# Kernel tuning notes

Measured on AMD Instinct MI355X. Metric: run time of the kernel, lower is better.

The kernel has to match this reference:

```python
import jax, jax.numpy as jnp
import numpy as np

N, M, D = 65536, 1024, 2


def setup_inputs() -> dict:
    key = jax.random.key(0)
    k1, k2, k3 = jax.random.split(key, 3)
    sample = jax.random.uniform(k1, (N, D), dtype=jnp.float32)
    mu = jax.random.uniform(k2, (M, D), dtype=jnp.float32)
    # original init: A = 10 * I; add small noise so covariances are anisotropic
    A = 10.0 * jnp.broadcast_to(jnp.eye(D, dtype=jnp.float32), (M, D, D)) \
        + 0.1 * jax.random.normal(k3, (M, D, D), dtype=jnp.float32)
    w = jnp.ones((M, 1), dtype=jnp.float32)
    return {"sample": sample, "mu": mu, "A": A, "w": w}


def reference(sample, mu, A, w):
    # gamma_j = A_j @ A_j^T  -> precision matrices, (M, D, D)
    gamma = jnp.einsum('mde,mfe->mdf', A, A)
    # 2x2 determinant (only case implemented in the original module)
    det = gamma[:, 0, 0] * gamma[:, 1, 1] - gamma[:, 0, 1] * gamma[:, 1, 0]
    # log weights: log_softmax(w) + 0.5 * log det(gamma)
    log_w = jax.nn.log_softmax(w[:, 0], axis=0) + 0.5 * jnp.log(det)  # (M,)
    # Mahalanobis quadratic form q_ij = (x_i - mu_j)^T gamma_j (x_i - mu_j),
    # expanded to avoid materializing an (N, M, D) difference tensor.
    xGx = jnp.einsum('nd,mde,ne->nm', sample, gamma, sample)          # (N, M)
    gm = jnp.einsum('mde,me->md', gamma, mu)                          # (M, D)
    cross = sample @ gm.T                                             # (N, M)
    mGm = jnp.einsum('md,md->m', gm, mu)                              # (M,)
    q = xGx - 2.0 * cross + mGm[None, :]
    # log-likelihood per sample: logsumexp_j (log_w_j - q_ij)
    return jax.nn.logsumexp(log_w[None, :] - q, axis=1)               # (N,)
```

## Files before the change

kernel.cpp:

```cpp
#include <hip/hip_runtime.h>
#include <math.h>

#define LOG2E 1.4426950408889634f
#define LN2   0.6931471805599453f

static constexpr int M = 1024;
static constexpr int N = 65536;

__device__ inline float wave_max64(float v) {
    #pragma unroll
    for (int o = 32; o > 0; o >>= 1) v = fmaxf(v, __shfl_xor(v, o));
    return v;
}
__device__ inline float wave_sum64(float v) {
    #pragma unroll
    for (int o = 32; o > 0; o >>= 1) v += __shfl_xor(v, o);
    return v;
}

__global__ __launch_bounds__(1024)
void gm_all(const float* __restrict__ sample,
            const float* __restrict__ mu,
            const float* __restrict__ A,
            const float* __restrict__ w,
            float* __restrict__ out) {
    __shared__ __align__(16) float coef[M*6];
    __shared__ float partial[16*256];
    __shared__ float redA[16];
    __shared__ float redB[16];

    const int t    = threadIdx.x;
    const int lane = t & 63;
    const int wv   = t >> 6;
    const int base = blockIdx.x * 256;

    float x0[4], x1[4];
    #pragma unroll
    for (int k = 0; k < 4; k++) {
        const float2 p = ((const float2*)sample)[base + 64*k + lane];
        x0[k] = p.x; x1[k] = p.y;
    }

    const float4 a = ((const float4*)A)[t];
    const float g00 = a.x*a.x + a.y*a.y;
    const float g01 = a.x*a.z + a.y*a.w;
    const float g11 = a.z*a.z + a.w*a.w;
    const float2 m  = ((const float2*)mu)[t];
    const float gm0 = g00*m.x + g01*m.y;
    const float gm1 = g01*m.x + g11*m.y;
    const float mGm = gm0*m.x + gm1*m.y;
    const float det = g00*g11 - g01*g01;

    const float w2 = w[t] * LOG2E;
    const float t2 = w2 + 0.5f * __builtin_amdgcn_logf(det);

    float mw = wave_max64(w2);
    float mt = wave_max64(t2);
    if (lane == 0) { redA[wv] = mw; redB[wv] = mt; }
    __syncthreads();
    float wmax2 = redA[0], maxt2 = redB[0];
    #pragma unroll
    for (int i = 1; i < 16; i++) {
        wmax2 = fmaxf(wmax2, redA[i]);
        maxt2 = fmaxf(maxt2, redB[i]);
    }

    {
        float* c = coef + t*6;
        c[0] = t2 - maxt2 - LOG2E * mGm;
        c[1] = LOG2E * 2.0f * gm0;
        c[2] = LOG2E * 2.0f * gm1;
        c[3] = -LOG2E * g00;
        c[4] = -LOG2E * 2.0f * g01;
        c[5] = -LOG2E * g11;
    }
    __syncthreads();

    float sw = wave_sum64(__builtin_amdgcn_exp2f(w2 - wmax2));
    if (lane == 0) redA[wv] = sw;

    const float xx[4] = {x0[0]*x0[0], x0[1]*x0[1], x0[2]*x0[2], x0[3]*x0[3]};
    const float xy[4] = {x0[0]*x1[0], x0[1]*x1[1], x0[2]*x1[2], x0[3]*x1[3]};
    const float yy[4] = {x1[0]*x1[0], x1[1]*x1[1], x1[2]*x1[2], x1[3]*x1[3]};
    float accA[4] = {0.0f, 0.0f, 0.0f, 0.0f};
    float accB[4] = {0.0f, 0.0f, 0.0f, 0.0f};

    const float4* cw = (const float4*)(coef + wv*64*6);
    #pragma unroll 8
    for (int jj = 0; jj < 32; jj++) {
        const float4 q0 = cw[jj*3 + 0];
        const float4 q1 = cw[jj*3 + 1];
        const float4 q2 = cw[jj*3 + 2];
        #pragma unroll
        for (int k = 0; k < 4; k++) {
            const float va = fmaf(q1.y, yy[k], fmaf(q1.x, xy[k],
                             fmaf(q0.w, xx[k], fmaf(q0.z, x1[k],
                             fmaf(q0.y, x0[k], q0.x)))));
            const float vb = fmaf(q2.w, yy[k], fmaf(q2.z, xy[k],
                             fmaf(q2.y, xx[k], fmaf(q2.x, x1[k],
                             fmaf(q1.w, x0[k], q1.z)))));
            accA[k] += __builtin_amdgcn_exp2f(va);
            accB[k] += __builtin_amdgcn_exp2f(vb);
        }
    }

    #pragma unroll
    for (int k = 0; k < 4; k++)
        partial[wv*256 + 64*k + lane] = accA[k] + accB[k];
    __syncthreads();

    if (t < 256) {
        float s = 0.0f;
        #pragma unroll
        for (int w2i = 0; w2i < 16; w2i++) s += partial[w2i*256 + t];
        float se = 0.0f;
        #pragma unroll
        for (int i = 0; i < 16; i++) se += redA[i];
        const float lse2 = wmax2 + __builtin_amdgcn_logf(se);
        out[base + t] = LN2 * (maxt2 - lse2 + __builtin_amdgcn_logf(s));
    }
}

extern "C" void kernel_launch(void* const* d_in, const int* in_sizes, int n_in,
                              void* d_out, int out_size, void* d_ws, size_t ws_size,
                              hipStream_t stream) {
    const float* sample = (const float*)d_in[0];
    const float* mu     = (const float*)d_in[1];
    const float* A      = (const float*)d_in[2];
    const float* w      = (const float*)d_in[3];
    float* out = (float*)d_out;
    (void)d_ws; (void)ws_size;

    gm_all<<<N/256, 1024, 0, stream>>>(sample, mu, A, w, out);
}
```

Before: 72.85 us.

## Split coefficient prep into separate kernel and use packed FP32 FMA

```diff
diff --git a/kernel.cpp b/kernel.cpp
--- a/kernel.cpp
+++ b/kernel.cpp
@@ -6,6 +6,14 @@
 
 static constexpr int M = 1024;
 static constexpr int N = 65536;
+
+typedef float v2f __attribute__((ext_vector_type(2)));
+
+__device__ inline v2f pk_fma(v2f a, v2f b, v2f c) {
+    v2f d;
+    asm("v_pk_fma_f32 %0, %1, %2, %3" : "=v"(d) : "v"(a), "v"(b), "v"(c));
+    return d;
+}
 
 __device__ inline float wave_max64(float v) {
     #pragma unroll
@@ -19,27 +27,15 @@
 }
 
 __global__ __launch_bounds__(1024)
-void gm_all(const float* __restrict__ sample,
-            const float* __restrict__ mu,
-            const float* __restrict__ A,
-            const float* __restrict__ w,
-            float* __restrict__ out) {
-    __shared__ __align__(16) float coef[M*6];
-    __shared__ float partial[16*256];
+void gm_prep(const float* __restrict__ mu,
+             const float* __restrict__ A,
+             const float* __restrict__ w,
+             float* __restrict__ ws) {
     __shared__ float redA[16];
     __shared__ float redB[16];
-
     const int t    = threadIdx.x;
     const int lane = t & 63;
     const int wv   = t >> 6;
-    const int base = blockIdx.x * 256;
-
-    float x0[4], x1[4];
-    #pragma unroll
-    for (int k = 0; k < 4; k++) {
-        const float2 p = ((const float2*)sample)[base + 64*k + lane];
-        x0[k] = p.x; x1[k] = p.y;
-    }
 
     const float4 a = ((const float4*)A)[t];
     const float g00 = a.x*a.x + a.y*a.y;
@@ -64,60 +60,93 @@
         wmax2 = fmaxf(wmax2, redA[i]);
         maxt2 = fmaxf(maxt2, redB[i]);
     }
+    __syncthreads();
+    const float sw = wave_sum64(__builtin_amdgcn_exp2f(w2 - wmax2));
+    if (lane == 0) redA[wv] = sw;
+
+    float* c = ws + (t >> 1)*12 + (t & 1);
+    c[0]  = t2 - maxt2 - LOG2E * mGm;
+    c[2]  = LOG2E * 2.0f * gm0;
+    c[4]  = LOG2E * 2.0f * gm1;
+    c[6]  = -LOG2E * g00;
+    c[8]  = -LOG2E * 2.0f * g01;
+    c[10] = -LOG2E * g11;
+
+    __syncthreads();
+    if (t == 0) {
+        float se = 0.0f;
+        #pragma unroll
+        for (int i = 0; i < 16; i++) se += redA[i];
+        ws[M*6] = maxt2 - (wmax2 + __builtin_amdgcn_logf(se));
+    }
+}
+
+__global__ __launch_bounds__(1024, 8)
+void gm_main(const float* __restrict__ sample,
+             const float* __restrict__ ws,
+             float* __restrict__ out) {
+    __shared__ __align__(16) float coef[M*6];
+    __shared__ float partial[16*128];
+
+    const int t    = threadIdx.x;
+    const int lane = t & 63;
+    const int wv   = t >> 6;
+    const int base = blockIdx.x * 128;
+
+    const float2 p0 = ((const float2*)sample)[base + lane];
+    const float2 p1 = ((const float2*)sample)[base + 64 + lane];
+
+    const float k_off = ws[M*6];
 
     {
-        float* c = coef + t*6;
-        c[0] = t2 - maxt2 - LOG2E * mGm;
-        c[1] = LOG2E * 2.0f * gm0;
-        c[2] = LOG2E * 2.0f * gm1;
-        c[3] = -LOG2E * g00;
-        c[4] = -LOG2E * 2.0f * g01;
-        c[5] = -LOG2E * g11;
+        const float2* src = (const float2*)ws;
+        float2* dst = (float2*)coef;
+        #pragma unroll
+        for (int i = 0; i < 3; i++) dst[t + 1024*i] = src[t + 1024*i];
     }
     __syncthreads();
 
-    float sw = wave_sum64(__builtin_amdgcn_exp2f(w2 - wmax2));
-    if (lane == 0) redA[wv] = sw;
+    const v2f X0  = {p0.x, p0.x},      Y0  = {p0.y, p0.y};
+    const v2f XX0 = {p0.x*p0.x, p0.x*p0.x};
+    const v2f XY0 = {p0.x*p0.y, p0.x*p0.y};
+    const v2f YY0 = {p0.y*p0.y, p0.y*p0.y};
+    const v2f X1  = {p1.x, p1.x},      Y1  = {p1.y, p1.y};
+    const v2f XX1 = {p1.x*p1.x, p1.x*p1.x};
+    const v2f XY1 = {p1.x*p1.y, p1.x*p1.y};
+    const v2f YY1 = {p1.y*p1.y, p1.y*p1.y};
 
-    const float xx[4] = {x0[0]*x0[0], x0[1]*x0[1], x0[2]*x0[2], x0[3]*x0[3]};
-    const float xy[4] = {x0[0]*x1[0], x0[1]*x1[1], x0[2]*x1[2], x0[3]*x1[3]};
-    const float yy[4] = {x1[0]*x1[0], x1[1]*x1[1], x1[2]*x1[2], x1[3]*x1[3]};
-    float accA[4] = {0.0f, 0.0f, 0.0f, 0.0f};
-    float accB[4] = {0.0f, 0.0f, 0.0f, 0.0f};
+    float acc0a = 0.0f, acc0b = 0.0f, acc1a = 0.0f, acc1b = 0.0f;
 
-    const float4* cw = (const float4*)(coef + wv*64*6);
-    #pragma unroll 8
+    const float4* cw = (const float4*)coef + wv*32*3;
+    #pragma unroll 4
     for (int jj = 0; jj < 32; jj++) {
         const float4 q0 = cw[jj*3 + 0];
         const float4 q1 = cw[jj*3 + 1];
         const float4 q2 = cw[jj*3 + 2];
-        #pragma unroll
-        for (int k = 0; k < 4; k++) {
-            const float va = fmaf(q1.y, yy[k], fmaf(q1.x, xy[k],
-                             fmaf(q0.w, xx[k], fmaf(q0.z, x1[k],
-                             fmaf(q0.y, x0[k], q0.x)))));
-            const float vb = fmaf(q2.w, yy[k], fmaf(q2.z, xy[k],
-                             fmaf(q2.y, xx[k], fmaf(q2.x, x1[k],
-                             fmaf(q1.w, x0[k], q1.z)))));
-            accA[k] += __builtin_amdgcn_exp2f(va);
-            accB[k] += __builtin_amdgcn_exp2f(vb);
-        }
+        const v2f c0 = {q0.x, q0.y}, c1 = {q0.z, q0.w};
+        const v2f c2 = {q1.x, q1.y}, c3 = {q1.z, q1.w};
+        const v2f c4 = {q2.x, q2.y}, c5 = {q2.z, q2.w};
+
+        v2f v0 = pk_fma(c5, YY0, pk_fma(c4, XY0, pk_fma(c3, XX0,
+                 pk_fma(c2, Y0,  pk_fma(c1, X0, c0)))));
+        v2f v1 = pk_fma(c5, YY1, pk_fma(c4, XY1, pk_fma(c3, XX1,
+                 pk_fma(c2, Y1,  pk_fma(c1, X1, c0)))));
+
+        acc0a += __builtin_amdgcn_exp2f(v0.x);
+        acc0b += __builtin_amdgcn_exp2f(v0.y);
+        acc1a += __builtin_amdgcn_exp2f(v1.x);
+        acc1b += __builtin_amdgcn_exp2f(v1.y);
     }
 
-    #pragma unroll
-    for (int k = 0; k < 4; k++)
-        partial[wv*256 + 64*k + lane] = accA[k] + accB[k];
+    partial[wv*128 + lane]      = acc0a + acc0b;
+    partial[wv*128 + 64 + lane] = acc1a + acc1b;
     __syncthreads();
 
-    if (t < 256) {
-        float s = 0.0f;
+    if (t < 128) {
+        float s = partial[t];
         #pragma unroll
-        for (int w2i = 0; w2i < 16; w2i++) s += partial[w2i*256 + t];
-        float se = 0.0f;
-        #pragma unroll
-        for (int i = 0; i < 16; i++) se += redA[i];
-        const float lse2 = wmax2 + __builtin_amdgcn_logf(se);
-        out[base + t] = LN2 * (maxt2 - lse2 + __builtin_amdgcn_logf(s));
+        for (int i = 1; i < 16; i++) s += partial[i*128 + t];
+        out[base + t] = LN2 * (k_off + __builtin_amdgcn_logf(s));
     }
 }
 
@@ -128,8 +157,8 @@
     const float* mu     = (const float*)d_in[1];
     const float* A      = (const float*)d_in[2];
     const float* w      = (const float*)d_in[3];
-    float* out = (float*)d_out;
-    (void)d_ws; (void)ws_size;
+    (void)in_sizes; (void)n_in; (void)out_size; (void)ws_size;
 
-    gm_all<<<N/256, 1024, 0, stream>>>(sample, mu, A, w, out);
+    gm_prep<<<1, 1024, 0, stream>>>(mu, A, w, (float*)d_ws);
+    gm_main<<<N/128, 1024, 0, stream>>>(sample, (const float*)d_ws, (float*)d_out);
 }
```

After: 74.56 us. 2.3% more time.

## Use packed FP32 FMA with Horner-form quadratic and drop block-wide max syncs

Applied to the files above, without the earlier changes.

```diff
diff --git a/kernel.cpp b/kernel.cpp
--- a/kernel.cpp
+++ b/kernel.cpp
@@ -6,6 +6,14 @@
 
 static constexpr int M = 1024;
 static constexpr int N = 65536;
+
+typedef float v2f __attribute__((ext_vector_type(2)));
+
+__device__ inline v2f pkfma(v2f a, v2f b, v2f c) {
+    v2f d;
+    asm("v_pk_fma_f32 %0, %1, %2, %3" : "=v"(d) : "v"(a), "v"(b), "v"(c));
+    return d;
+}
 
 __device__ inline float wave_max64(float v) {
     #pragma unroll
@@ -26,98 +34,106 @@
             float* __restrict__ out) {
     __shared__ __align__(16) float coef[M*6];
     __shared__ float partial[16*256];
-    __shared__ float redA[16];
-    __shared__ float redB[16];
 
     const int t    = threadIdx.x;
     const int lane = t & 63;
     const int wv   = t >> 6;
     const int base = blockIdx.x * 256;
 
-    float x0[4], x1[4];
+    float2 s[4];
     #pragma unroll
-    for (int k = 0; k < 4; k++) {
-        const float2 p = ((const float2*)sample)[base + 64*k + lane];
-        x0[k] = p.x; x1[k] = p.y;
+    for (int k = 0; k < 4; ++k)
+        s[k] = ((const float2*)sample)[base + 64*k + lane];
+
+    const float4 a4  = ((const float4*)A)[t];
+    const float2 mu2 = ((const float2*)mu)[t];
+    const float  wt  = w[t];
+
+    float4 wq[4];
+    #pragma unroll
+    for (int i = 0; i < 4; ++i)
+        wq[i] = ((const float4*)w)[lane + 64*i];
+
+    const float g00 = a4.x*a4.x + a4.y*a4.y;
+    const float g01 = a4.x*a4.z + a4.y*a4.w;
+    const float g11 = a4.z*a4.z + a4.w*a4.w;
+    const float gm0 = g00*mu2.x + g01*mu2.y;
+    const float gm1 = g01*mu2.x + g11*mu2.y;
+    const float mGm = gm0*mu2.x + gm1*mu2.y;
+    const float det = g00*g11 - g01*g01;
+    const float t2  = wt*LOG2E + 0.5f*__builtin_amdgcn_logf(det);
+
+    {
+        float* c = coef + (t >> 1)*12 + (t & 1);
+        c[0]  = t2 - LOG2E * mGm;
+        c[2]  = LOG2E * 2.0f * gm0;
+        c[4]  = LOG2E * 2.0f * gm1;
+        c[6]  = -LOG2E * g00;
+        c[8]  = -LOG2E * 2.0f * g01;
+        c[10] = -LOG2E * g11;
     }
 
-    const float4 a = ((const float4*)A)[t];
-    const float g00 = a.x*a.x + a.y*a.y;
-    const float g01 = a.x*a.z + a.y*a.w;
-    const float g11 = a.z*a.z + a.w*a.w;
-    const float2 m  = ((const float2*)mu)[t];
-    const float gm0 = g00*m.x + g01*m.y;
-    const float gm1 = g01*m.x + g11*m.y;
-    const float mGm = gm0*m.x + gm1*m.y;
-    const float det = g00*g11 - g01*g01;
+    float wmax = wq[0].x;
+    #pragma unroll
+    for (int i = 0; i < 4; ++i) {
+        wmax = fmaxf(wmax, wq[i].x); wmax = fmaxf(wmax, wq[i].y);
+        wmax = fmaxf(wmax, wq[i].z); wmax = fmaxf(wmax, wq[i].w);
+    }
+    wmax = wave_max64(wmax);
+    float sw = 0.0f;
+    #pragma unroll
+    for (int i = 0; i < 4; ++i) {
+        sw += __builtin_amdgcn_exp2f((wq[i].x - wmax)*LOG2E);
+        sw += __builtin_amdgcn_exp2f((wq[i].y - wmax)*LOG2E);
+        sw += __builtin_amdgcn_exp2f((wq[i].z - wmax)*LOG2E);
+        sw += __builtin_amdgcn_exp2f((wq[i].w - wmax)*LOG2E);
+    }
+    sw = wave_sum64(sw);
+    const float nlse = -(wmax*LOG2E + __builtin_amdgcn_logf(sw));
 
-    const float w2 = w[t] * LOG2E;
-    const float t2 = w2 + 0.5f * __builtin_amdgcn_logf(det);
+    asm volatile("s_waitcnt lgkmcnt(0)" ::: "memory");
+    __builtin_amdgcn_sched_barrier(0);
 
-    float mw = wave_max64(w2);
-    float mt = wave_max64(t2);
-    if (lane == 0) { redA[wv] = mw; redB[wv] = mt; }
-    __syncthreads();
-    float wmax2 = redA[0], maxt2 = redB[0];
+    v2f X[4], Y[4];
     #pragma unroll
-    for (int i = 1; i < 16; i++) {
-        wmax2 = fmaxf(wmax2, redA[i]);
-        maxt2 = fmaxf(maxt2, redB[i]);
+    for (int k = 0; k < 4; ++k) {
+        X[k] = (v2f){s[k].x, s[k].x};
+        Y[k] = (v2f){s[k].y, s[k].y};
     }
-
-    {
-        float* c = coef + t*6;
-        c[0] = t2 - maxt2 - LOG2E * mGm;
-        c[1] = LOG2E * 2.0f * gm0;
-        c[2] = LOG2E * 2.0f * gm1;
-        c[3] = -LOG2E * g00;
-        c[4] = -LOG2E * 2.0f * g01;
-        c[5] = -LOG2E * g11;
-    }
-    __syncthreads();
-
-    float sw = wave_sum64(__builtin_amdgcn_exp2f(w2 - wmax2));
-    if (lane == 0) redA[wv] = sw;
-
-    const float xx[4] = {x0[0]*x0[0], x0[1]*x0[1], x0[2]*x0[2], x0[3]*x0[3]};
-    const float xy[4] = {x0[0]*x1[0], x0[1]*x1[1], x0[2]*x1[2], x0[3]*x1[3]};
-    const float yy[4] = {x1[0]*x1[0], x1[1]*x1[1], x1[2]*x1[2], x1[3]*x1[3]};
-    float accA[4] = {0.0f, 0.0f, 0.0f, 0.0f};
-    float accB[4] = {0.0f, 0.0f, 0.0f, 0.0f};
+    v2f acc[4] = {(v2f){0,0},(v2f){0,0},(v2f){0,0},(v2f){0,0}};
 
     const float4* cw = (const float4*)(coef + wv*64*6);
-    #pragma unroll 8
-    for (int jj = 0; jj < 32; jj++) {
-        const float4 q0 = cw[jj*3 + 0];
-        const float4 q1 = cw[jj*3 + 1];
-        const float4 q2 = cw[jj*3 + 2];
+    #pragma unroll 4
+    for (int p = 0; p < 32; ++p) {
+        const float4 q0 = cw[p*3 + 0];
+        const float4 q1 = cw[p*3 + 1];
+        const float4 q2 = cw[p*3 + 2];
+        const v2f c0 = {q0.x, q0.y}, c1 = {q0.z, q0.w};
+        const v2f c2 = {q1.x, q1.y}, c3 = {q1.z, q1.w};
+        const v2f c4 = {q2.x, q2.y}, c5 = {q2.z, q2.w};
         #pragma unroll
-        for (int k = 0; k < 4; k++) {
-            const float va = fmaf(q1.y, yy[k], fmaf(q1.x, xy[k],
-                             fmaf(q0.w, xx[k], fmaf(q0.z, x1[k],
-                             fmaf(q0.y, x0[k], q0.x)))));
-            const float vb = fmaf(q2.w, yy[k], fmaf(q2.z, xy[k],
-                             fmaf(q2.y, xx[k], fmaf(q2.x, x1[k],
-                             fmaf(q1.w, x0[k], q1.z)))));
-            accA[k] += __builtin_amdgcn_exp2f(va);
-            accB[k] += __builtin_amdgcn_exp2f(vb);
+        for (int k = 0; k < 4; ++k) {
+            v2f u  = pkfma(c3, X[k], c1);
+            u      = pkfma(c4, Y[k], u);
+            v2f t3 = pkfma(c5, Y[k], c2);
+            v2f v  = pkfma(u,  X[k], c0);
+            v      = pkfma(t3, Y[k], v);
+            const float ea = __builtin_amdgcn_exp2f(fmaxf(v.x, -126.0f));
+            const float eb = __builtin_amdgcn_exp2f(fmaxf(v.y, -126.0f));
+            acc[k] += (v2f){ea, eb};
         }
     }
 
     #pragma unroll
-    for (int k = 0; k < 4; k++)
-        partial[wv*256 + 64*k + lane] = accA[k] + accB[k];
+    for (int k = 0; k < 4; ++k)
+        partial[wv*256 + 64*k + lane] = acc[k].x + acc[k].y;
     __syncthreads();
 
     if (t < 256) {
-        float s = 0.0f;
+        float ssum = partial[t];
         #pragma unroll
-        for (int w2i = 0; w2i < 16; w2i++) s += partial[w2i*256 + t];
-        float se = 0.0f;
-        #pragma unroll
-        for (int i = 0; i < 16; i++) se += redA[i];
-        const float lse2 = wmax2 + __builtin_amdgcn_logf(se);
-        out[base + t] = LN2 * (maxt2 - lse2 + __builtin_amdgcn_logf(s));
+        for (int i = 1; i < 16; ++i) ssum += partial[i*256 + t];
+        out[base + t] = LN2 * (nlse + __builtin_amdgcn_logf(ssum));
     }
 }
 
@@ -129,7 +145,7 @@
     const float* A      = (const float*)d_in[2];
     const float* w      = (const float*)d_in[3];
     float* out = (float*)d_out;
-    (void)d_ws; (void)ws_size;
+    (void)in_sizes; (void)n_in; (void)out_size; (void)d_ws; (void)ws_size;
 
-    gm_all<<<N/256, 1024, 0, stream>>>(sample, mu, A, w, out);
+    gm_all<<<256, 1024, 0, stream>>>(sample, mu, A, w, out);
 }
```

Measured after the change: 74.04 us. Within noise of the previous version (+1.6%).
